# Kernel optimization log

Hardware: AMD Instinct MI355X
Metric: run time of the kernel (lower is better)

The kernel has to match this reference:

```python
import jax, jax.numpy as jnp
import numpy as np

B, L = 64, 4096
NIN, NST = 8, 16
CIN = NIN + NST          # 24 input channels to FNO
WIDTH = 64               # hidden_channels
MODES = 32               # n_modes_height
NL = 4                   # n_layers
PROJ = 128               # projection hidden width (standard FNO1d)


def setup_inputs() -> dict:
    key = jax.random.key(0)
    ks = jax.random.split(key, 12)
    u = jax.random.normal(ks[0], (B, L, NIN), jnp.float32)
    z = jax.random.normal(ks[1], (B, NST), jnp.float32)
    t = jax.random.normal(ks[2], (B,), jnp.float32)
    # lifting
    fc0_w = jax.random.normal(ks[3], (CIN, WIDTH), jnp.float32) / np.sqrt(CIN)
    fc0_b = jnp.zeros((WIDTH,), jnp.float32)
    # spectral weights (real/imag parts) and 1x1 skip convs per layer
    scale = 1.0 / (WIDTH * WIDTH)
    spec_wr = scale * jax.random.normal(ks[4], (NL, WIDTH, WIDTH, MODES), jnp.float32)
    spec_wi = scale * jax.random.normal(ks[5], (NL, WIDTH, WIDTH, MODES), jnp.float32)
    skip_w = jax.random.normal(ks[6], (NL, WIDTH, WIDTH), jnp.float32) / np.sqrt(WIDTH)
    skip_b = jnp.zeros((NL, WIDTH), jnp.float32)
    # projection
    fc1_w = jax.random.normal(ks[7], (WIDTH, PROJ), jnp.float32) / np.sqrt(WIDTH)
    fc1_b = jnp.zeros((PROJ,), jnp.float32)
    fc2_w = jax.random.normal(ks[8], (PROJ, NST), jnp.float32) / np.sqrt(PROJ)
    fc2_b = jnp.zeros((NST,), jnp.float32)
    return dict(u=u, z=z, t=t, fc0_w=fc0_w, fc0_b=fc0_b,
                spec_wr=spec_wr, spec_wi=spec_wi, skip_w=skip_w, skip_b=skip_b,
                fc1_w=fc1_w, fc1_b=fc1_b, fc2_w=fc2_w, fc2_b=fc2_b)


def _fno_forward(x, fc0_w, fc0_b, spec_wr, spec_wi, skip_w, skip_b,
                 fc1_w, fc1_b, fc2_w, fc2_b):
    # x: [B, L, CIN]
    n = x.shape[1]
    h = jnp.einsum('blc,cw->blw', x, fc0_w) + fc0_b        # lift -> [B, L, W]
    h = jnp.transpose(h, (0, 2, 1))                         # [B, W, L] channels-first
    nfreq = n // 2 + 1
    for l in range(NL):
        hf = jnp.fft.rfft(h, axis=-1)                       # [B, W, nfreq] complex
        wc = (spec_wr[l] + 1j * spec_wi[l]).astype(hf.dtype)  # [W, W, M]
        of = jnp.einsum('bim,iom->bom', hf[..., :MODES], wc)  # truncated-mode matmul
        full = jnp.zeros(h.shape[:2] + (nfreq,), hf.dtype).at[..., :MODES].set(of)
        spec = jnp.fft.irfft(full, n=n, axis=-1)            # [B, W, L]
        skip = jnp.einsum('bil,io->bol', h, skip_w[l]) + skip_b[l][None, :, None]
        h = spec + skip
        if l < NL - 1:
            h = jax.nn.gelu(h)
    h = jnp.transpose(h, (0, 2, 1))                         # [B, L, W]
    q = jax.nn.gelu(jnp.einsum('blw,wp->blp', h, fc1_w) + fc1_b)
    return jnp.einsum('blp,po->blo', q, fc2_w) + fc2_b      # [B, L, NST]


def reference(u, z, t, fc0_w, fc0_b, spec_wr, spec_wi, skip_w, skip_b,
              fc1_w, fc1_b, fc2_w, fc2_b):
    # z.tile(seq_len).reshape(B, seq_len, n_state) == broadcast along time
    rep_z = jnp.broadcast_to(z[:, None, :], (z.shape[0], u.shape[1], z.shape[1]))
    x = jnp.concatenate([u, rep_z], axis=-1)                # [B, L, CIN]
    outs = _fno_forward(x, fc0_w, fc0_b, spec_wr, spec_wi, skip_w, skip_b,
                        fc1_w, fc1_b, fc2_w, fc2_b)         # [B, L, NST]
    return outs[:, -1, :]                                   # [B, NST]
```

## Files before the change

### kernel.cpp

```cpp
#include <hip/hip_runtime.h>
#include <math.h>

#define LL 4096
#define NB 64
#define WW 64
#define NMODES 32
#define NCIN 24
#define NLAY 4
#define NPROJ 128
#define NSTC 16
#define NSPLIT 16

static __device__ __forceinline__ float gelu_tanh(float x){
    const float c0 = 0.7978845608028654f;
    const float c1 = 0.044715f;
    float t = tanhf(c0*(x + c1*x*x*x));
    return 0.5f*x*(1.0f+t);
}

__global__ void k_tables(float* __restrict__ TD, float* __restrict__ TI){
    int idx = blockIdx.x*256 + threadIdx.x;
    if (idx >= LL*NMODES) return;
    int x = idx & (LL-1);
    int k = idx >> 12;
    int ph = (k*x) & (LL-1);
    float ang = (6.283185307179586f/(float)LL)*(float)ph;
    float c = cosf(ang), s = sinf(ang);
    TD[(size_t)k*LL + x] = c;
    TD[(size_t)(k+NMODES)*LL + x] = -s;
    if (k == 0){
        TI[x] = 1.0f/(float)LL;
        TI[(size_t)NMODES*LL + x] = 0.0f;
    } else {
        TI[(size_t)k*LL + x] = (2.0f/(float)LL)*c;
        TI[(size_t)(k+NMODES)*LL + x] = -(2.0f/(float)LL)*s;
    }
}

__global__ void k_wt(const float* __restrict__ wr, const float* __restrict__ wi,
                     float* __restrict__ wrT, float* __restrict__ wiT){
    int idx = blockIdx.x*256 + threadIdx.x;
    if (idx >= NLAY*WW*WW*NMODES) return;
    int m = idx & 31;
    int o = (idx >> 5) & 63;
    int i = (idx >> 11) & 63;
    int l = idx >> 17;
    size_t dst = (((size_t)l*NMODES + m)*WW + i)*WW + o;
    wrT[dst] = wr[idx];
    wiT[dst] = wi[idx];
}

__global__ void k_lift(const float* __restrict__ u, const float* __restrict__ z,
                       const float* __restrict__ w0, const float* __restrict__ b0,
                       float* __restrict__ h){
    __shared__ float Ws[NCIN*WW];
    __shared__ float Bs[WW];
    __shared__ float Zs[16];
    int b = blockIdx.y;
    int x0 = blockIdx.x*256;
    int tid = threadIdx.x;
    for (int i = tid; i < NCIN*WW; i += 256) Ws[i] = w0[i];
    if (tid < WW) Bs[tid] = b0[tid];
    if (tid < 16) Zs[tid] = z[b*16 + tid];
    __syncthreads();
    int x = x0 + tid;
    const float4* up = (const float4*)(u + ((size_t)b*LL + x)*8);
    float4 a0 = up[0], a1 = up[1];
    float ur[8] = {a0.x,a0.y,a0.z,a0.w,a1.x,a1.y,a1.z,a1.w};
    float zr[16];
    #pragma unroll
    for (int j=0;j<16;j++) zr[j] = Zs[j];
    for (int c=0;c<WW;c++){
        float acc = Bs[c];
        #pragma unroll
        for (int j=0;j<8;j++)  acc += ur[j]*Ws[j*WW+c];
        #pragma unroll
        for (int j=0;j<16;j++) acc += zr[j]*Ws[(8+j)*WW+c];
        h[((size_t)b*WW + c)*LL + x] = acc;
    }
}

__global__ void k_dft(const float* __restrict__ h, const float* __restrict__ TD,
                      float* __restrict__ part){
    __shared__ float Ah[64*68];
    __shared__ float Tn[64*68];
    int rt = blockIdx.x;
    int s  = blockIdx.y;
    int tid = threadIdx.x;
    int rowBase = rt*64;
    int rg = tid >> 3;
    int j  = tid & 7;
    float acc[2][8];
    #pragma unroll
    for (int i=0;i<2;i++)
        #pragma unroll
        for (int q=0;q<8;q++) acc[i][q] = 0.f;

    for (int kc=0; kc<256; kc+=64){
        int kb = s*256 + kc;
        __syncthreads();
        #pragma unroll
        for (int t=0;t<4;t++){
            int f = tid + t*256;
            int rr = f >> 4, xo = (f & 15)*4;
            *(float4*)&Ah[rr*68 + xo] = *(const float4*)(h + (size_t)(rowBase+rr)*LL + kb + xo);
        }
        #pragma unroll
        for (int t=0;t<4;t++){
            int f = tid + t*256;
            int nn = f >> 4, xo = (f & 15)*4;
            *(float4*)&Tn[nn*68 + xo] = *(const float4*)(TD + (size_t)nn*LL + kb + xo);
        }
        __syncthreads();
        for (int kk=0; kk<64; kk+=4){
            float a[2][4];
            #pragma unroll
            for (int i=0;i<2;i++){
                float4 t = *(const float4*)&Ah[(rg+32*i)*68 + kk];
                a[i][0]=t.x; a[i][1]=t.y; a[i][2]=t.z; a[i][3]=t.w;
            }
            float tn[8][4];
            #pragma unroll
            for (int q=0;q<8;q++){
                float4 t = *(const float4*)&Tn[(j+8*q)*68 + kk];
                tn[q][0]=t.x; tn[q][1]=t.y; tn[q][2]=t.z; tn[q][3]=t.w;
            }
            #pragma unroll
            for (int d=0;d<4;d++)
                #pragma unroll
                for (int i=0;i<2;i++)
                    #pragma unroll
                    for (int q=0;q<8;q++)
                        acc[i][q] += a[i][d]*tn[q][d];
        }
    }
    #pragma unroll
    for (int i=0;i<2;i++)
        #pragma unroll
        for (int q=0;q<8;q++)
            part[((size_t)s*4096 + rowBase + rg + 32*i)*64 + j + 8*q] = acc[i][q];
}

__global__ void k_reduce(const float* __restrict__ part, float* __restrict__ hfT){
    int e = blockIdx.x*256 + threadIdx.x;
    int i    = e & 63;
    int reim = (e >> 6) & 1;
    int m    = (e >> 7) & 31;
    int b    = e >> 12;
    int n = m + 32*reim;
    size_t rowoff = ((size_t)b*WW + i)*64 + n;
    float s = 0.f;
    #pragma unroll
    for (int sp=0; sp<NSPLIT; sp++) s += part[(size_t)sp*262144 + rowoff];
    hfT[e] = s;
}

__global__ void k_mix(const float* __restrict__ hfT, const float* __restrict__ wrT,
                      const float* __restrict__ wiT, float* __restrict__ of){
    int m = blockIdx.x, b = blockIdx.y;
    int o = threadIdx.x;
    __shared__ float hr[64], hi[64];
    const float* row = hfT + ((size_t)b*NMODES + m)*128;
    hr[o] = row[o];
    hi[o] = row[64+o];
    __syncthreads();
    float ar = 0.f, ai = 0.f;
    const float* wr = wrT + (size_t)m*4096;
    const float* wi = wiT + (size_t)m*4096;
    for (int i=0;i<64;i++){
        float wrv = wr[i*64+o], wiv = wi[i*64+o];
        float r = hr[i], im = hi[i];
        ar += r*wrv - im*wiv;
        ai += r*wiv + im*wrv;
    }
    of[((size_t)b*WW+o)*64 + m]      = ar;
    of[((size_t)b*WW+o)*64 + 32 + m] = ai;
}

__global__ void k_fused(const float* __restrict__ h, const float* __restrict__ of,
                        const float* __restrict__ skw, const float* __restrict__ skb,
                        const float* __restrict__ TI, float* __restrict__ hout,
                        int do_gelu){
    __shared__ float As[64*132];
    __shared__ float Bs[32*136];
    int b  = blockIdx.y;
    int x0 = blockIdx.x*128;
    int tid = threadIdx.x;
    for (int f = tid; f < 64*64; f += 256){
        int kk = f >> 6, o = f & 63;
        As[o*132 + kk] = skw[f];
    }
    for (int f = tid; f < 64*64; f += 256){
        int o = f >> 6, j = f & 63;
        As[o*132 + 64 + j] = of[((size_t)b*WW + o)*64 + j];
    }
    int og = tid >> 4, xg = tid & 15;
    int o0 = og*4, xt = xg*4;
    float acc[4][8];
    #pragma unroll
    for (int i=0;i<4;i++)
        #pragma unroll
        for (int e=0;e<8;e++) acc[i][e] = 0.f;

    for (int kc = 0; kc < 128; kc += 32){
        __syncthreads();
        for (int f = tid; f < 32*32; f += 256){
            int rr = f >> 5;
            int xo4 = f & 31;
            int g = kc + rr;
            const float* src = (g < 64) ? (h  + ((size_t)b*WW + g)*LL + x0 + xo4*4)
                                        : (TI + (size_t)(g-64)*LL   + x0 + xo4*4);
            *(float4*)&Bs[rr*136 + xo4*4] = *(const float4*)src;
        }
        __syncthreads();
        for (int kk = 0; kk < 32; kk += 4){
            float a[4][4];
            #pragma unroll
            for (int i=0;i<4;i++){
                float4 t = *(const float4*)&As[(o0+i)*132 + kc + kk];
                a[i][0]=t.x; a[i][1]=t.y; a[i][2]=t.z; a[i][3]=t.w;
            }
            #pragma unroll
            for (int d=0;d<4;d++){
                float4 b0 = *(const float4*)&Bs[(kk+d)*136 + xt];
                float4 b1 = *(const float4*)&Bs[(kk+d)*136 + xt + 64];
                float bb[8] = {b0.x,b0.y,b0.z,b0.w,b1.x,b1.y,b1.z,b1.w};
                #pragma unroll
                for (int i=0;i<4;i++)
                    #pragma unroll
                    for (int e=0;e<8;e++)
                        acc[i][e] += a[i][d]*bb[e];
            }
        }
    }
    #pragma unroll
    for (int i=0;i<4;i++){
        int o = o0+i;
        float bias = skb[o];
        #pragma unroll
        for (int e=0;e<8;e++){
            float v = acc[i][e] + bias;
            if (do_gelu) v = gelu_tanh(v);
            acc[i][e] = v;
        }
        size_t base = ((size_t)b*WW + o)*LL + x0 + xt;
        *(float4*)&hout[base]      = make_float4(acc[i][0],acc[i][1],acc[i][2],acc[i][3]);
        *(float4*)&hout[base + 64] = make_float4(acc[i][4],acc[i][5],acc[i][6],acc[i][7]);
    }
}

__global__ void k_final(const float* __restrict__ h3, const float* __restrict__ of,
                        const float* __restrict__ skw, const float* __restrict__ skb,
                        const float* __restrict__ TI,
                        const float* __restrict__ w1, const float* __restrict__ b1,
                        const float* __restrict__ w2, const float* __restrict__ b2,
                        float* __restrict__ out){
    int b = blockIdx.x;
    int tid = threadIdx.x;
    __shared__ float hch[64];
    __shared__ float til[64];
    __shared__ float hv[64];
    __shared__ float qv[128];
    if (tid < 64) hch[tid] = h3[((size_t)b*WW + tid)*LL + (LL-1)];
    else          til[tid-64] = TI[(size_t)(tid-64)*LL + (LL-1)];
    __syncthreads();
    if (tid < 64){
        int o = tid;
        float acc = skb[o];
        const float* ofr = of + ((size_t)b*WW + o)*64;
        #pragma unroll
        for (int j=0;j<64;j++) acc += ofr[j]*til[j];
        #pragma unroll
        for (int i=0;i<64;i++) acc += hch[i]*skw[i*64+o];
        hv[o] = acc;
    }
    __syncthreads();
    {
        int p = tid;
        float acc = b1[p];
        for (int o=0;o<64;o++) acc += hv[o]*w1[o*NPROJ+p];
        qv[p] = gelu_tanh(acc);
    }
    __syncthreads();
    if (tid < NSTC){
        int s = tid;
        float acc = b2[s];
        for (int p=0;p<NPROJ;p++) acc += qv[p]*w2[p*NSTC+s];
        out[b*NSTC + s] = acc;
    }
}

extern "C" void kernel_launch(void* const* d_in, const int* in_sizes, int n_in,
                              void* d_out, int out_size, void* d_ws, size_t ws_size,
                              hipStream_t stream) {
    const float* u     = (const float*)d_in[0];
    const float* z     = (const float*)d_in[1];
    const float* fc0w  = (const float*)d_in[3];
    const float* fc0b  = (const float*)d_in[4];
    const float* swr   = (const float*)d_in[5];
    const float* swi   = (const float*)d_in[6];
    const float* skw   = (const float*)d_in[7];
    const float* skb   = (const float*)d_in[8];
    const float* fc1w  = (const float*)d_in[9];
    const float* fc1b  = (const float*)d_in[10];
    const float* fc2w  = (const float*)d_in[11];
    const float* fc2b  = (const float*)d_in[12];
    float* out = (float*)d_out;

    const size_t SZ_H    = (size_t)NB*WW*LL*4;
    const size_t SZ_TD   = (size_t)64*LL*4;
    const size_t SZ_TI   = SZ_TD;
    const size_t SZ_PART = (size_t)NSPLIT*4096*64*4;
    const size_t SZ_HFT  = (size_t)64*32*128*4;
    const size_t SZ_OF   = (size_t)64*64*64*4;
    const size_t SZ_WT   = (size_t)NLAY*NMODES*WW*WW*4;

    size_t need = 2*SZ_H + SZ_TD + SZ_TI + SZ_PART + SZ_HFT + SZ_OF + 2*SZ_WT;
    if (ws_size < need) return;

    char* p = (char*)d_ws;
    float* hA   = (float*)p; p += SZ_H;
    float* hB   = (float*)p; p += SZ_H;
    float* TD   = (float*)p; p += SZ_TD;
    float* TI   = (float*)p; p += SZ_TI;
    float* part = (float*)p; p += SZ_PART;
    float* hfT  = (float*)p; p += SZ_HFT;
    float* of   = (float*)p; p += SZ_OF;
    float* wrT  = (float*)p; p += SZ_WT;
    float* wiT  = (float*)p; p += SZ_WT;

    k_tables<<<(LL*NMODES+255)/256, 256, 0, stream>>>(TD, TI);
    k_wt<<<(NLAY*WW*WW*NMODES+255)/256, 256, 0, stream>>>(swr, swi, wrT, wiT);
    k_lift<<<dim3(LL/256, NB), 256, 0, stream>>>(u, z, fc0w, fc0b, hA);

    float* hcur = hA;
    float* hnxt = hB;
    for (int l = 0; l < NLAY; l++){
        k_dft<<<dim3(64, NSPLIT), 256, 0, stream>>>(hcur, TD, part);
        k_reduce<<<(64*32*128)/256, 256, 0, stream>>>(part, hfT);
        k_mix<<<dim3(NMODES, NB), 64, 0, stream>>>(hfT, wrT + (size_t)l*NMODES*WW*WW,
                                                   wiT + (size_t)l*NMODES*WW*WW, of);
        if (l < NLAY-1){
            k_fused<<<dim3(LL/128, NB), 256, 0, stream>>>(hcur, of,
                skw + (size_t)l*WW*WW, skb + (size_t)l*WW, TI, hnxt, 1);
            float* tmp = hcur; hcur = hnxt; hnxt = tmp;
        }
    }
    k_final<<<NB, 128, 0, stream>>>(hcur, of, skw + (size_t)3*WW*WW, skb + (size_t)3*WW,
                                    TI, fc1w, fc1b, fc2w, fc2b, out);
}
```

Baseline: 622.3 us.

## Use split-bf16 MFMA for DFT and fused skip/inverse-DFT matmuls

```diff
diff --git a/kernel.cpp b/kernel.cpp
--- a/kernel.cpp
+++ b/kernel.cpp
@@ -10,6 +10,10 @@
 #define NPROJ 128
 #define NSTC 16
 #define NSPLIT 16
+#define PK 136
+
+typedef __attribute__((ext_vector_type(8))) short short8;
+typedef __attribute__((ext_vector_type(4))) float f32x4;
 
 static __device__ __forceinline__ float gelu_tanh(float x){
     const float c0 = 0.7978845608028654f;
@@ -18,7 +22,23 @@
     return 0.5f*x*(1.0f+t);
 }
 
-__global__ void k_tables(float* __restrict__ TD, float* __restrict__ TI){
+static __device__ __forceinline__ unsigned short bf16_rn(float v){
+    unsigned int u = __float_as_uint(v);
+    unsigned int r = (u + 0x7fffu + ((u>>16)&1u)) >> 16;
+    return (unsigned short)r;
+}
+static __device__ __forceinline__ float bf16f(unsigned short h){
+    return __uint_as_float(((unsigned int)h)<<16);
+}
+static __device__ __forceinline__ void split_store(unsigned short* hi, unsigned short* lo,
+                                                   size_t idx, float v){
+    unsigned short h = bf16_rn(v);
+    hi[idx] = h;
+    lo[idx] = bf16_rn(v - bf16f(h));
+}
+
+__global__ void k_tables(unsigned short* __restrict__ TD_hi, unsigned short* __restrict__ TD_lo,
+                         unsigned short* __restrict__ TI_hi, unsigned short* __restrict__ TI_lo){
     int idx = blockIdx.x*256 + threadIdx.x;
     if (idx >= LL*NMODES) return;
     int x = idx & (LL-1);
@@ -26,33 +46,41 @@
     int ph = (k*x) & (LL-1);
     float ang = (6.283185307179586f/(float)LL)*(float)ph;
     float c = cosf(ang), s = sinf(ang);
-    TD[(size_t)k*LL + x] = c;
-    TD[(size_t)(k+NMODES)*LL + x] = -s;
-    if (k == 0){
-        TI[x] = 1.0f/(float)LL;
-        TI[(size_t)NMODES*LL + x] = 0.0f;
-    } else {
-        TI[(size_t)k*LL + x] = (2.0f/(float)LL)*c;
-        TI[(size_t)(k+NMODES)*LL + x] = -(2.0f/(float)LL)*s;
-    }
+    split_store(TD_hi, TD_lo, (size_t)k*LL + x, c);
+    split_store(TD_hi, TD_lo, (size_t)(k+NMODES)*LL + x, -s);
+    float tc, ts;
+    if (k == 0){ tc = 1.0f/(float)LL; ts = 0.0f; }
+    else { tc = (2.0f/(float)LL)*c; ts = -(2.0f/(float)LL)*s; }
+    split_store(TI_hi, TI_lo, (size_t)k*LL + x, tc);
+    split_store(TI_hi, TI_lo, (size_t)(k+NMODES)*LL + x, ts);
 }
 
 __global__ void k_wt(const float* __restrict__ wr, const float* __restrict__ wi,
-                     float* __restrict__ wrT, float* __restrict__ wiT){
+                     float* __restrict__ wrT, float* __restrict__ wiT,
+                     const float* __restrict__ skw,
+                     unsigned short* __restrict__ skwT_hi, unsigned short* __restrict__ skwT_lo){
     int idx = blockIdx.x*256 + threadIdx.x;
-    if (idx >= NLAY*WW*WW*NMODES) return;
-    int m = idx & 31;
-    int o = (idx >> 5) & 63;
-    int i = (idx >> 11) & 63;
-    int l = idx >> 17;
-    size_t dst = (((size_t)l*NMODES + m)*WW + i)*WW + o;
-    wrT[dst] = wr[idx];
-    wiT[dst] = wi[idx];
+    if (idx < NLAY*WW*WW*NMODES){
+        int m = idx & 31;
+        int o = (idx >> 5) & 63;
+        int i = (idx >> 11) & 63;
+        int l = idx >> 17;
+        size_t dst = (((size_t)l*NMODES + m)*WW + i)*WW + o;
+        wrT[dst] = wr[idx];
+        wiT[dst] = wi[idx];
+    }
+    if (idx < NLAY*WW*WW){
+        int o = idx & 63;
+        int i = (idx >> 6) & 63;
+        int l = idx >> 12;
+        float v = skw[((size_t)l*WW + i)*WW + o];
+        split_store(skwT_hi, skwT_lo, ((size_t)l*WW + o)*WW + i, v);
+    }
 }
 
 __global__ void k_lift(const float* __restrict__ u, const float* __restrict__ z,
                        const float* __restrict__ w0, const float* __restrict__ b0,
-                       float* __restrict__ h){
+                       unsigned short* __restrict__ h_hi, unsigned short* __restrict__ h_lo){
     __shared__ float Ws[NCIN*WW];
     __shared__ float Bs[WW];
     __shared__ float Zs[16];
@@ -76,69 +104,46 @@
         for (int j=0;j<8;j++)  acc += ur[j]*Ws[j*WW+c];
         #pragma unroll
         for (int j=0;j<16;j++) acc += zr[j]*Ws[(8+j)*WW+c];
-        h[((size_t)b*WW + c)*LL + x] = acc;
-    }
-}
-
-__global__ void k_dft(const float* __restrict__ h, const float* __restrict__ TD,
-                      float* __restrict__ part){
-    __shared__ float Ah[64*68];
-    __shared__ float Tn[64*68];
+        split_store(h_hi, h_lo, ((size_t)b*WW + c)*LL + x, acc);
+    }
+}
+
+__global__ __launch_bounds__(256) void k_dft(
+        const unsigned short* __restrict__ h_hi, const unsigned short* __restrict__ h_lo,
+        const unsigned short* __restrict__ td_hi, const unsigned short* __restrict__ td_lo,
+        float* __restrict__ part){
     int rt = blockIdx.x;
     int s  = blockIdx.y;
     int tid = threadIdx.x;
-    int rowBase = rt*64;
-    int rg = tid >> 3;
-    int j  = tid & 7;
-    float acc[2][8];
-    #pragma unroll
-    for (int i=0;i<2;i++)
-        #pragma unroll
-        for (int q=0;q<8;q++) acc[i][q] = 0.f;
-
-    for (int kc=0; kc<256; kc+=64){
-        int kb = s*256 + kc;
-        __syncthreads();
-        #pragma unroll
-        for (int t=0;t<4;t++){
-            int f = tid + t*256;
-            int rr = f >> 4, xo = (f & 15)*4;
-            *(float4*)&Ah[rr*68 + xo] = *(const float4*)(h + (size_t)(rowBase+rr)*LL + kb + xo);
+    int w = tid >> 6;
+    int lane = tid & 63;
+    int g = lane >> 4;
+    int i = lane & 15;
+    f32x4 acc[4];
+    #pragma unroll
+    for (int nf=0;nf<4;nf++) acc[nf] = (f32x4){0.f,0.f,0.f,0.f};
+    size_t arow = (size_t)(rt*64 + w*16 + i)*LL;
+    int xbase = s*256;
+    for (int ks=0; ks<8; ks++){
+        int xk = xbase + ks*32 + g*8;
+        short8 a_hi = *(const short8*)(h_hi + arow + xk);
+        short8 a_lo = *(const short8*)(h_lo + arow + xk);
+        #pragma unroll
+        for (int nf=0;nf<4;nf++){
+            size_t brow = (size_t)(nf*16 + i)*LL + xk;
+            short8 b_hi = *(const short8*)(td_hi + brow);
+            short8 b_lo = *(const short8*)(td_lo + brow);
+            acc[nf] = __builtin_amdgcn_mfma_f32_16x16x32_bf16(a_lo, b_hi, acc[nf], 0,0,0);
+            acc[nf] = __builtin_amdgcn_mfma_f32_16x16x32_bf16(a_hi, b_lo, acc[nf], 0,0,0);
+            acc[nf] = __builtin_amdgcn_mfma_f32_16x16x32_bf16(a_hi, b_hi, acc[nf], 0,0,0);
         }
-        #pragma unroll
-        for (int t=0;t<4;t++){
-            int f = tid + t*256;
-            int nn = f >> 4, xo = (f & 15)*4;
-            *(float4*)&Tn[nn*68 + xo] = *(const float4*)(TD + (size_t)nn*LL + kb + xo);
-        }
-        __syncthreads();
-        for (int kk=0; kk<64; kk+=4){
-            float a[2][4];
-            #pragma unroll
-            for (int i=0;i<2;i++){
-                float4 t = *(const float4*)&Ah[(rg+32*i)*68 + kk];
-                a[i][0]=t.x; a[i][1]=t.y; a[i][2]=t.z; a[i][3]=t.w;
-            }
-            float tn[8][4];
-            #pragma unroll
-            for (int q=0;q<8;q++){
-                float4 t = *(const float4*)&Tn[(j+8*q)*68 + kk];
-                tn[q][0]=t.x; tn[q][1]=t.y; tn[q][2]=t.z; tn[q][3]=t.w;
-            }
-            #pragma unroll
-            for (int d=0;d<4;d++)
-                #pragma unroll
-                for (int i=0;i<2;i++)
-                    #pragma unroll
-                    for (int q=0;q<8;q++)
-                        acc[i][q] += a[i][d]*tn[q][d];
-        }
-    }
-    #pragma unroll
-    for (int i=0;i<2;i++)
-        #pragma unroll
-        for (int q=0;q<8;q++)
-            part[((size_t)s*4096 + rowBase + rg + 32*i)*64 + j + 8*q] = acc[i][q];
+    }
+    int drow = rt*64 + w*16 + g*4;
+    #pragma unroll
+    for (int nf=0;nf<4;nf++)
+        #pragma unroll
+        for (int r=0;r<4;r++)
+            part[((size_t)s*4096 + drow + r)*64 + nf*16 + i] = acc[nf][r];
 }
 
 __global__ void k_reduce(const float* __restrict__ part, float* __restrict__ hfT){
@@ -156,102 +161,135 @@
 }
 
 __global__ void k_mix(const float* __restrict__ hfT, const float* __restrict__ wrT,
-                      const float* __restrict__ wiT, float* __restrict__ of){
+                      const float* __restrict__ wiT, float* __restrict__ of,
+                      unsigned short* __restrict__ of_hi, unsigned short* __restrict__ of_lo){
     int m = blockIdx.x, b = blockIdx.y;
     int o = threadIdx.x;
-    __shared__ float hr[64], hi[64];
+    __shared__ float hr[64], hi_[64];
     const float* row = hfT + ((size_t)b*NMODES + m)*128;
     hr[o] = row[o];
-    hi[o] = row[64+o];
+    hi_[o] = row[64+o];
     __syncthreads();
     float ar = 0.f, ai = 0.f;
     const float* wr = wrT + (size_t)m*4096;
     const float* wi = wiT + (size_t)m*4096;
     for (int i=0;i<64;i++){
         float wrv = wr[i*64+o], wiv = wi[i*64+o];
-        float r = hr[i], im = hi[i];
+        float r = hr[i], im = hi_[i];
         ar += r*wrv - im*wiv;
         ai += r*wiv + im*wrv;
     }
-    of[((size_t)b*WW+o)*64 + m]      = ar;
-    of[((size_t)b*WW+o)*64 + 32 + m] = ai;
-}
-
-__global__ void k_fused(const float* __restrict__ h, const float* __restrict__ of,
+    size_t base = ((size_t)b*WW+o)*64;
+    of[base + m]      = ar;
+    of[base + 32 + m] = ai;
+    split_store(of_hi, of_lo, base + m, ar);
+    split_store(of_hi, of_lo, base + 32 + m, ai);
+}
+
+__global__ __launch_bounds__(256) void k_fused(
+        const unsigned short* __restrict__ h_hi, const unsigned short* __restrict__ h_lo,
+        const unsigned short* __restrict__ ti_hi, const unsigned short* __restrict__ ti_lo,
+        const unsigned short* __restrict__ skwT_hi, const unsigned short* __restrict__ skwT_lo,
+        const unsigned short* __restrict__ of_hi, const unsigned short* __restrict__ of_lo,
+        const float* __restrict__ skb,
+        unsigned short* __restrict__ ho_hi, unsigned short* __restrict__ ho_lo){
+    __shared__ __align__(16) char ldsraw[2*64*PK*2];
+    unsigned short* Bs_hi = (unsigned short*)ldsraw;
+    unsigned short* Bs_lo = Bs_hi + 64*PK;
+    int b  = blockIdx.y;
+    int X0 = blockIdx.x*64;
+    int tid = threadIdx.x;
+    int xl = tid & 63;
+    int kq = tid >> 6;
+    for (int pl=0; pl<2; pl++){
+        const unsigned short* hsrc = pl ? h_lo : h_hi;
+        const unsigned short* tsrc = pl ? ti_lo : ti_hi;
+        unsigned short* Bs = pl ? Bs_lo : Bs_hi;
+        #pragma unroll
+        for (int it=0; it<8; it++){
+            int k0 = (kq + it*4)*4;
+            const unsigned short* s0 = (k0 < 64)
+                ? (hsrc + ((size_t)(b*64 + k0))*LL + X0 + xl)
+                : (tsrc + ((size_t)(k0-64))*LL + X0 + xl);
+            unsigned short v0 = s0[0], v1 = s0[LL], v2 = s0[2*LL], v3 = s0[3*LL];
+            unsigned long long pk = (unsigned long long)v0
+                                  | ((unsigned long long)v1<<16)
+                                  | ((unsigned long long)v2<<32)
+                                  | ((unsigned long long)v3<<48);
+            *(unsigned long long*)(Bs + xl*PK + k0) = pk;
+        }
+    }
+    __syncthreads();
+    int w = tid >> 6, lane = tid & 63, g = lane >> 4, j = lane & 15;
+    f32x4 acc[4];
+    #pragma unroll
+    for (int mf=0; mf<4; mf++) acc[mf] = (f32x4){0.f,0.f,0.f,0.f};
+    const unsigned short* BrH = Bs_hi + (w*16 + j)*PK;
+    const unsigned short* BrL = Bs_lo + (w*16 + j)*PK;
+    #pragma unroll
+    for (int ks=0; ks<4; ks++){
+        short8 bh = *(const short8*)(BrH + ks*32 + g*8);
+        short8 bl = *(const short8*)(BrL + ks*32 + g*8);
+        #pragma unroll
+        for (int mf=0; mf<4; mf++){
+            int o = mf*16 + j;
+            const unsigned short *pa_hi, *pa_lo;
+            if (ks < 2){
+                pa_hi = skwT_hi + (o<<6) + ks*32 + g*8;
+                pa_lo = skwT_lo + (o<<6) + ks*32 + g*8;
+            } else {
+                size_t bo = ((size_t)(b*64 + o))<<6;
+                pa_hi = of_hi + bo + (ks-2)*32 + g*8;
+                pa_lo = of_lo + bo + (ks-2)*32 + g*8;
+            }
+            short8 ah = *(const short8*)pa_hi;
+            short8 al = *(const short8*)pa_lo;
+            acc[mf] = __builtin_amdgcn_mfma_f32_16x16x32_bf16(al, bh, acc[mf], 0,0,0);
+            acc[mf] = __builtin_amdgcn_mfma_f32_16x16x32_bf16(ah, bl, acc[mf], 0,0,0);
+            acc[mf] = __builtin_amdgcn_mfma_f32_16x16x32_bf16(ah, bh, acc[mf], 0,0,0);
+        }
+    }
+    __syncthreads();
+    unsigned int* T = (unsigned int*)ldsraw;
+    #pragma unroll
+    for (int mf=0; mf<4; mf++){
+        #pragma unroll
+        for (int r=0; r<4; r++){
+            int o = mf*16 + g*4 + r;
+            float v = acc[mf][r] + skb[o];
+            v = gelu_tanh(v);
+            unsigned short h16 = bf16_rn(v);
+            unsigned short l16 = bf16_rn(v - bf16f(h16));
+            T[o*65 + w*16 + j] = (unsigned int)h16 | ((unsigned int)l16 << 16);
+        }
+    }
+    __syncthreads();
+    #pragma unroll
+    for (int q=0; q<4; q++){
+        int f = tid + q*256;
+        int o = f >> 4, seg = f & 15;
+        const unsigned int* tr = T + o*65 + seg*4;
+        unsigned int t0=tr[0], t1=tr[1], t2=tr[2], t3=tr[3];
+        unsigned long long hv = (unsigned long long)(t0 & 0xffffu)
+            | ((unsigned long long)(t1 & 0xffffu)<<16)
+            | ((unsigned long long)(t2 & 0xffffu)<<32)
+            | ((unsigned long long)(t3 & 0xffffu)<<48);
+        unsigned long long lv = (unsigned long long)(t0 >> 16)
+            | ((unsigned long long)(t1 >> 16)<<16)
+            | ((unsigned long long)(t2 >> 16)<<32)
+            | ((unsigned long long)(t3 >> 16)<<48);
+        size_t base = ((size_t)(b*64 + o))*LL + X0 + seg*4;
+        *(unsigned long long*)(ho_hi + base) = hv;
+        *(unsigned long long*)(ho_lo + base) = lv;
+    }
+}
+
+__global__ void k_final(const unsigned short* __restrict__ h3_hi,
+                        const unsigned short* __restrict__ h3_lo,
+                        const float* __restrict__ of,
                         const float* __restrict__ skw, const float* __restrict__ skb,
-                        const float* __restrict__ TI, float* __restrict__ hout,
-                        int do_gelu){
-    __shared__ float As[64*132];
-    __shared__ float Bs[32*136];
-    int b  = blockIdx.y;
-    int x0 = blockIdx.x*128;
-    int tid = threadIdx.x;
-    for (int f = tid; f < 64*64; f += 256){
-        int kk = f >> 6, o = f & 63;
-        As[o*132 + kk] = skw[f];
-    }
-    for (int f = tid; f < 64*64; f += 256){
-        int o = f >> 6, j = f & 63;
-        As[o*132 + 64 + j] = of[((size_t)b*WW + o)*64 + j];
-    }
-    int og = tid >> 4, xg = tid & 15;
-    int o0 = og*4, xt = xg*4;
-    float acc[4][8];
-    #pragma unroll
-    for (int i=0;i<4;i++)
-        #pragma unroll
-        for (int e=0;e<8;e++) acc[i][e] = 0.f;
-
-    for (int kc = 0; kc < 128; kc += 32){
-        __syncthreads();
-        for (int f = tid; f < 32*32; f += 256){
-            int rr = f >> 5;
-            int xo4 = f & 31;
-            int g = kc + rr;
-            const float* src = (g < 64) ? (h  + ((size_t)b*WW + g)*LL + x0 + xo4*4)
-                                        : (TI + (size_t)(g-64)*LL   + x0 + xo4*4);
-            *(float4*)&Bs[rr*136 + xo4*4] = *(const float4*)src;
-        }
-        __syncthreads();
-        for (int kk = 0; kk < 32; kk += 4){
-            float a[4][4];
-            #pragma unroll
-            for (int i=0;i<4;i++){
-                float4 t = *(const float4*)&As[(o0+i)*132 + kc + kk];
-                a[i][0]=t.x; a[i][1]=t.y; a[i][2]=t.z; a[i][3]=t.w;
-            }
-            #pragma unroll
-            for (int d=0;d<4;d++){
-                float4 b0 = *(const float4*)&Bs[(kk+d)*136 + xt];
-                float4 b1 = *(const float4*)&Bs[(kk+d)*136 + xt + 64];
-                float bb[8] = {b0.x,b0.y,b0.z,b0.w,b1.x,b1.y,b1.z,b1.w};
-                #pragma unroll
-                for (int i=0;i<4;i++)
-                    #pragma unroll
-                    for (int e=0;e<8;e++)
-                        acc[i][e] += a[i][d]*bb[e];
-            }
-        }
-    }
-    #pragma unroll
-    for (int i=0;i<4;i++){
-        int o = o0+i;
-        float bias = skb[o];
-        #pragma unroll
-        for (int e=0;e<8;e++){
-            float v = acc[i][e] + bias;
-            if (do_gelu) v = gelu_tanh(v);
-            acc[i][e] = v;
-        }
-        size_t base = ((size_t)b*WW + o)*LL + x0 + xt;
-        *(float4*)&hout[base]      = make_float4(acc[i][0],acc[i][1],acc[i][2],acc[i][3]);
-        *(float4*)&hout[base + 64] = make_float4(acc[i][4],acc[i][5],acc[i][6],acc[i][7]);
-    }
-}
-
-__global__ void k_final(const float* __restrict__ h3, const float* __restrict__ of,
-                        const float* __restrict__ skw, const float* __restrict__ skb,
-                        const float* __restrict__ TI,
+                        const unsigned short* __restrict__ ti_hi,
+                        const unsigned short* __restrict__ ti_lo,
                         const float* __restrict__ w1, const float* __restrict__ b1,
                         const float* __restrict__ w2, const float* __restrict__ b2,
                         float* __restrict__ out){
@@ -261,8 +299,13 @@
     __shared__ float til[64];
     __shared__ float hv[64];
     __shared__ float qv[128];
-    if (tid < 64) hch[tid] = h3[((size_t)b*WW + tid)*LL + (LL-1)];
-    else          til[tid-64] = TI[(size_t)(tid-64)*LL + (LL-1)];
+    if (tid < 64){
+        size_t idx = ((size_t)(b*64 + tid))*LL + (LL-1);
+        hch[tid] = bf16f(h3_hi[idx]) + bf16f(h3_lo[idx]);
+    } else {
+        size_t idx = (size_t)(tid-64)*LL + (LL-1);
+        til[tid-64] = bf16f(ti_hi[idx]) + bf16f(ti_lo[idx]);
+    }
     __syncthreads();
     if (tid < 64){
         int o = tid;
@@ -307,45 +350,59 @@
     const float* fc2b  = (const float*)d_in[12];
     float* out = (float*)d_out;
 
-    const size_t SZ_H    = (size_t)NB*WW*LL*4;
-    const size_t SZ_TD   = (size_t)64*LL*4;
-    const size_t SZ_TI   = SZ_TD;
-    const size_t SZ_PART = (size_t)NSPLIT*4096*64*4;
+    const size_t SZ_HP   = (size_t)4096*LL*2;
+    const size_t SZ_TBL  = (size_t)64*LL*2;
     const size_t SZ_HFT  = (size_t)64*32*128*4;
     const size_t SZ_OF   = (size_t)64*64*64*4;
+    const size_t SZ_OFP  = (size_t)64*64*64*2;
     const size_t SZ_WT   = (size_t)NLAY*NMODES*WW*WW*4;
-
-    size_t need = 2*SZ_H + SZ_TD + SZ_TI + SZ_PART + SZ_HFT + SZ_OF + 2*SZ_WT;
+    const size_t SZ_SKT  = (size_t)NLAY*WW*WW*2;
+
+    size_t need = 4*SZ_HP + 4*SZ_TBL + SZ_HFT + SZ_OF + 2*SZ_OFP + 2*SZ_WT + 2*SZ_SKT;
     if (ws_size < need) return;
 
     char* p = (char*)d_ws;
-    float* hA   = (float*)p; p += SZ_H;
-    float* hB   = (float*)p; p += SZ_H;
-    float* TD   = (float*)p; p += SZ_TD;
-    float* TI   = (float*)p; p += SZ_TI;
-    float* part = (float*)p; p += SZ_PART;
-    float* hfT  = (float*)p; p += SZ_HFT;
-    float* of   = (float*)p; p += SZ_OF;
-    float* wrT  = (float*)p; p += SZ_WT;
-    float* wiT  = (float*)p; p += SZ_WT;
-
-    k_tables<<<(LL*NMODES+255)/256, 256, 0, stream>>>(TD, TI);
-    k_wt<<<(NLAY*WW*WW*NMODES+255)/256, 256, 0, stream>>>(swr, swi, wrT, wiT);
-    k_lift<<<dim3(LL/256, NB), 256, 0, stream>>>(u, z, fc0w, fc0b, hA);
-
-    float* hcur = hA;
-    float* hnxt = hB;
+    unsigned short* hA_hi = (unsigned short*)p; p += SZ_HP;
+    unsigned short* hA_lo = (unsigned short*)p; p += SZ_HP;
+    unsigned short* hB_hi = (unsigned short*)p; p += SZ_HP;
+    unsigned short* hB_lo = (unsigned short*)p; p += SZ_HP;
+    unsigned short* TD_hi = (unsigned short*)p; p += SZ_TBL;
+    unsigned short* TD_lo = (unsigned short*)p; p += SZ_TBL;
+    unsigned short* TI_hi = (unsigned short*)p; p += SZ_TBL;
+    unsigned short* TI_lo = (unsigned short*)p; p += SZ_TBL;
+    float* hfT   = (float*)p; p += SZ_HFT;
+    float* of    = (float*)p; p += SZ_OF;
+    unsigned short* of_hi = (unsigned short*)p; p += SZ_OFP;
+    unsigned short* of_lo = (unsigned short*)p; p += SZ_OFP;
+    float* wrT   = (float*)p; p += SZ_WT;
+    float* wiT   = (float*)p; p += SZ_WT;
+    unsigned short* skwT_hi = (unsigned short*)p; p += SZ_SKT;
+    unsigned short* skwT_lo = (unsigned short*)p; p += SZ_SKT;
+
+    k_tables<<<(LL*NMODES+255)/256, 256, 0, stream>>>(TD_hi, TD_lo, TI_hi, TI_lo);
+    k_wt<<<(NLAY*WW*WW*NMODES+255)/256, 256, 0, stream>>>(swr, swi, wrT, wiT,
+                                                          skw, skwT_hi, skwT_lo);
+    k_lift<<<dim3(LL/256, NB), 256, 0, stream>>>(u, z, fc0w, fc0b, hA_hi, hA_lo);
+
+    unsigned short* cur_hi = hA_hi; unsigned short* cur_lo = hA_lo;
+    unsigned short* nxt_hi = hB_hi; unsigned short* nxt_lo = hB_lo;
     for (int l = 0; l < NLAY; l++){
-        k_dft<<<dim3(64, NSPLIT), 256, 0, stream>>>(hcur, TD, part);
+        float* part = (float*)nxt_hi;
+        k_dft<<<dim3(64, NSPLIT), 256, 0, stream>>>(cur_hi, cur_lo, TD_hi, TD_lo, part);
         k_reduce<<<(64*32*128)/256, 256, 0, stream>>>(part, hfT);
         k_mix<<<dim3(NMODES, NB), 64, 0, stream>>>(hfT, wrT + (size_t)l*NMODES*WW*WW,
-                                                   wiT + (size_t)l*NMODES*WW*WW, of);
+                                                   wiT + (size_t)l*NMODES*WW*WW,
+                                                   of, of_hi, of_lo);
         if (l < NLAY-1){
-            k_fused<<<dim3(LL/128, NB), 256, 0, stream>>>(hcur, of,
-                skw + (size_t)l*WW*WW, skb + (size_t)l*WW, TI, hnxt, 1);
-            float* tmp = hcur; hcur = hnxt; hnxt = tmp;
+            k_fused<<<dim3(LL/64, NB), 256, 0, stream>>>(cur_hi, cur_lo, TI_hi, TI_lo,
+                skwT_hi + (size_t)l*WW*WW, skwT_lo + (size_t)l*WW*WW,
+                of_hi, of_lo, skb + (size_t)l*WW, nxt_hi, nxt_lo);
+            unsigned short* t;
+            t = cur_hi; cur_hi = nxt_hi; nxt_hi = t;
+            t = cur_lo; cur_lo = nxt_lo; nxt_lo = t;
         }
     }
-    k_final<<<NB, 128, 0, stream>>>(hcur, of, skw + (size_t)3*WW*WW, skb + (size_t)3*WW,
-                                    TI, fc1w, fc1b, fc2w, fc2b, out);
-}
+    k_final<<<NB, 128, 0, stream>>>(cur_hi, cur_lo, of, skw + (size_t)3*WW*WW,
+                                    skb + (size_t)3*WW, TI_hi, TI_lo,
+                                    fc1w, fc1b, fc2w, fc2b, out);
+}
```

Measured after the change: 657.1 us. +5.6%, slower.
